# Kernel optimization log

Measured on AMD Instinct MI355X. Metric: run time of the kernel, lower is better.

The kernel has to match this reference:

```python
import jax
import jax.numpy as jnp
import numpy as np
import math

KNN = 16
DIST_THRESH = 0.03


def setup_inputs() -> dict:
    key = jax.random.key(0)
    ks = jax.random.split(key, 7)
    B, N, M = 2, 8192, 8192
    Din, D = 64, 64
    feature1 = jax.random.normal(ks[0], (B, N, Din), dtype=jnp.float32)
    xyz1 = jax.random.uniform(ks[1], (B, N, 3), dtype=jnp.float32)
    xyz2 = jax.random.uniform(ks[2], (B, M, 3), dtype=jnp.float32)
    Wp = jax.random.normal(ks[3], (Din, D), dtype=jnp.float32) * 0.05
    bp = jnp.zeros((D,), dtype=jnp.float32)
    W1 = jax.random.normal(ks[4], (3, D), dtype=jnp.float32) * 0.05
    b1 = jnp.zeros((D,), dtype=jnp.float32)
    W2 = jax.random.normal(ks[5], (D, D), dtype=jnp.float32) * 0.05
    b2 = jnp.zeros((D,), dtype=jnp.float32)
    return {"feature1": feature1, "xyz1": xyz1, "xyz2": xyz2,
            "Wp": Wp, "bp": bp, "W1": W1, "b1": b1, "W2": W2, "b2": b2}


def reference(feature1, xyz1, xyz2, Wp, bp, W1, b1, W2, b2):
    # prefix linear: [B,N,Din] -> [B,N,D]
    f = feature1 @ Wp + bp

    # knn_point: squared pairwise distance from queries xyz2 to points xyz1
    # d2: [B, M, N]
    d2 = (jnp.sum(xyz2 * xyz2, axis=-1)[:, :, None]
          + jnp.sum(xyz1 * xyz1, axis=-1)[:, None, :]
          - 2.0 * jnp.einsum('bmd,bnd->bmn', xyz2, xyz1))
    neg_d, idx = jax.lax.top_k(-d2, KNN)        # smallest-k, ascending
    dist = -neg_d                                # [B, M, KNN]

    min_distance = dist[:, :, 0]                 # [B, M]
    weight = jnp.where(min_distance > DIST_THRESH, 10.0, 1.0).astype(f.dtype)

    # index_points: per-batch gather of neighbor features / coords
    g_feature = jax.vmap(lambda a, i: a[i])(f, idx)      # [B, M, KNN, D]
    g_xyz = jax.vmap(lambda a, i: a[i])(xyz1, idx)       # [B, M, KNN, 3]
    g_xyz = g_xyz - xyz2[:, :, None, :]                  # relative coords

    # fc_position MLP: 3 -> D -> D
    pw = jax.nn.relu(g_xyz @ W1 + b1) @ W2 + b2          # [B, M, KNN, D]

    # per-channel weighted reduction over KNN neighbors
    new_feature = jnp.einsum('bmkc,bmkc->bmc', pw, g_feature) / math.sqrt(KNN)
    return new_feature, weight
```

## Files before the change

### kernel.cpp

```cpp
#include <hip/hip_runtime.h>
#include <math.h>

#define B 2
#define N 8192
#define M 8192
#define D 64
#define KNN 16
#define BM (B * M)
#define GC 16
#define NC (GC * GC * GC)
#define NSC 64
#define WTMAX 192
#define CAP 20
#define TCAP 448

using frag_ab = __attribute__((ext_vector_type(8))) short;
using frag_cd = __attribute__((ext_vector_type(4))) float;

__device__ __forceinline__ short f2bf(float x) {
    unsigned u = __float_as_uint(x);
    u += 0x7fffu + ((u >> 16) & 1u);
    return (short)(u >> 16);
}

__device__ __forceinline__ float query_cutr(float qx, float qy, float qz) {
    int nc = ((qx < 0.16f) | (qx > 0.84f)) + ((qy < 0.16f) | (qy > 0.84f))
           + ((qz < 0.16f) | (qz > 0.84f));
    return nc == 0 ? 0.121f : nc == 1 ? 0.1525f : nc == 2 ? 0.1921f : 0.242f;
}

#define CHAIN_INS(VARR, IARR, DVAL, IVAL) do {                          \
    float _dd = (DVAL); int _ii = (IVAL);                               \
    _Pragma("unroll")                                                   \
    for (int _r = 0; _r < KNN; ++_r) {                                  \
        bool  _sm = _dd < VARR[_r];                                     \
        float _tv = VARR[_r]; int _ti = IARR[_r];                       \
        VARR[_r] = _sm ? _dd : _tv;  IARR[_r] = _sm ? _ii : _ti;        \
        _dd      = _sm ? _tv : _dd;  _ii      = _sm ? _ti : _ii;        \
    }                                                                   \
} while (0)
#define CHAIN_INSERT(DVAL, IVAL) CHAIN_INS(v, id, DVAL, IVAL)

#define BITONIC_ROUND(VARR, IARR, DL) do {                              \
    float _nv[KNN]; int _nid[KNN];                                      \
    _Pragma("unroll")                                                   \
    for (int _i = 0; _i < KNN; ++_i) {                                  \
        float _pv = __shfl_xor(VARR[KNN - 1 - _i], (DL), 64);           \
        int   _pi = __shfl_xor(IARR[KNN - 1 - _i], (DL), 64);           \
        bool _tk = VARR[_i] <= _pv;                                     \
        _nv[_i]  = _tk ? VARR[_i] : _pv;                                \
        _nid[_i] = _tk ? IARR[_i] : _pi;                                \
    }                                                                   \
    _Pragma("unroll")                                                   \
    for (int _st = 8; _st; _st >>= 1) {                                 \
        _Pragma("unroll")                                               \
        for (int _i = 0; _i < KNN; ++_i) {                              \
            if (!(_i & _st)) {                                          \
                int _j = _i | _st;                                      \
                bool _sw = _nv[_i] > _nv[_j];                           \
                float _ta = _sw ? _nv[_j] : _nv[_i];                    \
                float _tb = _sw ? _nv[_i] : _nv[_j];                    \
                int _ia = _sw ? _nid[_j] : _nid[_i];                    \
                int _ib = _sw ? _nid[_i] : _nid[_j];                    \
                _nv[_i] = _ta; _nv[_j] = _tb;                           \
                _nid[_i] = _ia; _nid[_j] = _ib;                         \
            }                                                           \
        }                                                               \
    }                                                                   \
    _Pragma("unroll")                                                   \
    for (int _i = 0; _i < KNN; ++_i) { VARR[_i] = _nv[_i]; IARR[_i] = _nid[_i]; } \
} while (0)

#define KPROC(PV, TV) do {                                              \
    float _dx = (PV).x - qx, _dy = (PV).y - qy, _dz = (PV).z - qz;      \
    float _dv = fmaf(_dx, _dx, fmaf(_dy, _dy, _dz * _dz));              \
    if (_dv < fcut) {                                                   \
        if (cnt < CAP) {                                                \
            ibuf[cnt][lane] = (unsigned short)(TV);                     \
            ++cnt;                                                      \
        } else {                                   \
            CHAIN_INSERT(_dv, __float_as_int((PV).w));                  \
        }                                                               \
    }                                                                   \
} while (0)

#define KFLUSH() do {                                                   \
    int _t = 0;                                                         \
    for (; _t + 4 <= cur; _t += 4) {                                    \
        float4 _q0 = tile[_t + 0], _q1 = tile[_t + 1];                  \
        float4 _q2 = tile[_t + 2], _q3 = tile[_t + 3];                  \
        KPROC(_q0, _t + 0); KPROC(_q1, _t + 1);                         \
        KPROC(_q2, _t + 2); KPROC(_q3, _t + 3);                         \
    }                                                                   \
    for (; _t < cur; ++_t) { float4 _q0 = tile[_t]; KPROC(_q0, _t); }   \
    int _mx = cnt;                                                      \
    _Pragma("unroll")                                                   \
    for (int _o = 32; _o; _o >>= 1)                                     \
        _mx = max(_mx, __shfl_xor(_mx, _o, 64));                        \
    _mx = __builtin_amdgcn_readfirstlane(_mx);                          \
    int _t2 = 0;                                                        \
    for (; _t2 + 2 <= _mx; _t2 += 2) {                                  \
        int _ta = (_t2     < cnt) ? (int)ibuf[_t2    ][lane] : 0;       \
        int _tb = (_t2 + 1 < cnt) ? (int)ibuf[_t2 + 1][lane] : 0;       \
        float4 _pa = tile[_ta], _pb = tile[_tb];   \
        float _dxa = _pa.x - qx, _dya = _pa.y - qy, _dza = _pa.z - qz;  \
        float _dva = fmaf(_dxa, _dxa, fmaf(_dya, _dya, _dza * _dza));   \
        if (_t2 < cnt && _dva < v[KNN - 1])                             \
            CHAIN_INSERT(_dva, __float_as_int(_pa.w));                  \
        float _dxb = _pb.x - qx, _dyb = _pb.y - qy, _dzb = _pb.z - qz;  \
        float _dvb = fmaf(_dxb, _dxb, fmaf(_dyb, _dyb, _dzb * _dzb));   \
        if (_t2 + 1 < cnt && _dvb < v[KNN - 1])                         \
            CHAIN_INSERT(_dvb, __float_as_int(_pb.w));                  \
    }                                                                   \
    for (; _t2 < _mx; ++_t2) {                                          \
        int _tp = (_t2 < cnt) ? (int)ibuf[_t2][lane] : 0;               \
        float4 _p = tile[_tp];                                          \
        float _dx = _p.x - qx, _dy = _p.y - qy, _dz = _p.z - qz;        \
        float _dv = fmaf(_dx, _dx, fmaf(_dy, _dy, _dz * _dz));          \
        if (_t2 < cnt && _dv < v[KNN - 1])                              \
            CHAIN_INSERT(_dv, __float_as_int(_p.w));                    \
    }                                                                   \
    cnt = 0; cur = 0;                                                   \
} while (0)

__global__ __launch_bounds__(256) void k_prep(const float* __restrict__ feat,
                                              const float* __restrict__ Wp,
                                              const float* __restrict__ bp,
                                              const float* __restrict__ xyz1,
                                              const float* __restrict__ xyz2,
                                              unsigned* __restrict__ pcount,
                                              unsigned* __restrict__ qcount,
                                              float* __restrict__ f) {
    if (blockIdx.x < 64) {
        int i = blockIdx.x * 256 + threadIdx.x;
        int b = i >> 13;
        const float* p = xyz1 + (size_t)i * 3;
        int cx = max(0, min(GC - 1, (int)(p[0] * GC)));
        int cy = max(0, min(GC - 1, (int)(p[1] * GC)));
        int cz = max(0, min(GC - 1, (int)(p[2] * GC)));
        atomicAdd(&pcount[b * NC + (cz * GC + cy) * GC + cx], 1u);
        const float* q = xyz2 + (size_t)i * 3;
        int qx = max(0, min(GC - 1, (int)(q[0] * GC)));
        int qy = max(0, min(GC - 1, (int)(q[1] * GC)));
        int qz = max(0, min(GC - 1, (int)(q[2] * GC)));
        int sc = ((qz >> 2) * 4 + (qy >> 2)) * 4 + (qx >> 2);
        atomicAdd(&qcount[b * NSC + sc], 1u);
    }
    int c  = threadIdx.x & 63;
    int wv = threadIdx.x >> 6;
    int row0 = blockIdx.x * 32 + wv * 8;
    float wp[64];
#pragma unroll
    for (int d = 0; d < 64; ++d) wp[d] = Wp[d * 64 + c];
    float bpc = bp[c];
    float fv[8], acc[8];
#pragma unroll
    for (int r = 0; r < 8; ++r) {
        fv[r]  = feat[(size_t)(row0 + r) * 64 + c];
        acc[r] = bpc;
    }
#pragma unroll
    for (int d = 0; d < 64; ++d) {
#pragma unroll
        for (int r = 0; r < 8; ++r)
            acc[r] = fmaf(__shfl(fv[r], d, 64), wp[d], acc[r]);
    }
#pragma unroll
    for (int r = 0; r < 8; ++r)
        f[(size_t)(row0 + r) * 64 + c] = acc[r];
}

__global__ __launch_bounds__(256) void k_scan(const unsigned* __restrict__ pcount,
                                              const unsigned* __restrict__ qcount,
                                              unsigned* __restrict__ pstart,
                                              unsigned* __restrict__ pcur,
                                              unsigned* __restrict__ qcur,
                                              int* __restrict__ wtab,
                                              int* __restrict__ ntab) {
    __shared__ unsigned wsum[4];
    int blk = blockIdx.x;
    if (blk < 2) {
        int b = blk;
        int t = threadIdx.x;
        int base = b * NC + t * 16;
        unsigned c[16]; unsigned tsum = 0;
#pragma unroll
        for (int k = 0; k < 16; ++k) { c[k] = pcount[base + k]; tsum += c[k]; }
        int lane = t & 63, wv = t >> 6;
        unsigned x = tsum;
#pragma unroll
        for (int off = 1; off < 64; off <<= 1) {
            unsigned y = __shfl_up(x, off, 64);
            if (lane >= off) x += y;
        }
        if (lane == 63) wsum[wv] = x;
        __syncthreads();
        unsigned pre = 0;
        for (int k2 = 0; k2 < wv; ++k2) pre += wsum[k2];
        unsigned run = pre + x - tsum;
#pragma unroll
        for (int k = 0; k < 16; ++k) {
            pstart[base + k] = run; pcur[base + k] = run; run += c[k];
        }
    } else {
        int b = blk - 2;
        if (threadIdx.x >= 64) return;
        int lane = threadIdx.x;
        int c = (int)qcount[b * NSC + lane];
        int x = c;
#pragma unroll
        for (int off = 1; off < 64; off <<= 1) {
            int y = __shfl_up(x, off, 64);
            if (lane >= off) x += y;
        }
        int run = x - c;
        qcur[b * NSC + lane] = (unsigned)run;
        int ne = (c + 63) >> 6;
        int e = ne;
#pragma unroll
        for (int off = 1; off < 64; off <<= 1) {
            int y = __shfl_up(e, off, 64);
            if (lane >= off) e += y;
        }
        int eoff = e - ne;
        for (int j = 0; j < ne; ++j)
            wtab[b * WTMAX + eoff + j] = ((run + j * 64) << 7) | min(64, c - j * 64);
        if (lane == 63) ntab[b] = eoff + ne;
    }
}

__global__ __launch_bounds__(256) void k_scatter(const float* __restrict__ xyz1,
                                                 const float* __restrict__ xyz2,
                                                 unsigned* __restrict__ pcur,
                                                 unsigned* __restrict__ qcur,
                                                 float4* __restrict__ spts,
                                                 int* __restrict__ sidx,
                                                 float4* __restrict__ squery) {
    int i = blockIdx.x * 256 + threadIdx.x;
    int b = i >> 13;
    const float* p = xyz1 + (size_t)i * 3;
    float x = p[0], y = p[1], z = p[2];
    int cx = max(0, min(GC - 1, (int)(x * GC)));
    int cy = max(0, min(GC - 1, (int)(y * GC)));
    int cz = max(0, min(GC - 1, (int)(z * GC)));
    unsigned pos = atomicAdd(&pcur[b * NC + (cz * GC + cy) * GC + cx], 1u);
    spts[(size_t)b * N + pos] = make_float4(x, y, z, fmaf(x, x, fmaf(y, y, z * z)));
    sidx[(size_t)b * N + pos] = i & (N - 1);

    const float* q = xyz2 + (size_t)i * 3;
    float qx = q[0], qy = q[1], qz = q[2];
    int ax = max(0, min(GC - 1, (int)(qx * GC)));
    int ay = max(0, min(GC - 1, (int)(qy * GC)));
    int az = max(0, min(GC - 1, (int)(qz * GC)));
    int sc = ((az >> 2) * 4 + (ay >> 2)) * 4 + (ax >> 2);
    unsigned qpos = atomicAdd(&qcur[b * NSC + sc], 1u);
    squery[(size_t)b * M + qpos] = make_float4(qx, qy, qz, __int_as_float(i));
}

template <int NSLT>
__global__ __launch_bounds__(64) void k_knn(const float4* __restrict__ spts,
                                            const float4* __restrict__ squery,
                                            const unsigned* __restrict__ pstart,
                                            const unsigned* __restrict__ pcount,
                                            const int* __restrict__ wtab,
                                            const int* __restrict__ ntab,
                                            float* __restrict__ part_d,
                                            int* __restrict__ part_i) {
    __shared__ float4         tile[TCAP];
    __shared__ unsigned short ibuf[CAP][64];
    int bid = blockIdx.x;
    int b   = bid / (WTMAX * NSLT);
    int rem = bid - b * (WTMAX * NSLT);
    int ti  = rem / NSLT;
    int s   = rem % NSLT;
    if (ti >= ntab[b]) return;
    int e = wtab[b * WTMAX + ti];
    int qnum = e & 127, qoff = (e >> 7) & 0x3FFF;
    int lane = threadIdx.x;

    int sl = lane < qnum ? lane : qnum - 1;
    float4 q4 = squery[(size_t)b * M + qoff + sl];
    float qx = q4.x, qy = q4.y, qz = q4.z;
    float cutr = query_cutr(qx, qy, qz);
    float fcut = cutr * cutr;

    int lx0 = max(0, (int)floorf((qx - cutr) * GC));
    int lx1 = min(GC - 1, (int)floorf((qx + cutr) * GC));
    int ly0 = max(0, (int)floorf((qy - cutr) * GC));
    int ly1 = min(GC - 1, (int)floorf((qy + cutr) * GC));
    int lz0 = max(0, (int)floorf((qz - cutr) * GC));
    int lz1 = min(GC - 1, (int)floorf((qz + cutr) * GC));
#pragma unroll
    for (int off = 1; off < 64; off <<= 1) {
        lx0 = min(lx0, __shfl_xor(lx0, off, 64));
        lx1 = max(lx1, __shfl_xor(lx1, off, 64));
        ly0 = min(ly0, __shfl_xor(ly0, off, 64));
        ly1 = max(ly1, __shfl_xor(ly1, off, 64));
        lz0 = min(lz0, __shfl_xor(lz0, off, 64));
        lz1 = max(lz1, __shfl_xor(lz1, off, 64));
    }
    int bx0 = __builtin_amdgcn_readfirstlane(lx0);
    int bx1 = __builtin_amdgcn_readfirstlane(lx1);
    int by0 = __builtin_amdgcn_readfirstlane(ly0);
    int by1 = __builtin_amdgcn_readfirstlane(ly1);
    int bz0 = __builtin_amdgcn_readfirstlane(lz0);
    int bz1 = __builtin_amdgcn_readfirstlane(lz1);

    float v[KNN]; int id[KNN];
#pragma unroll
    for (int r = 0; r < KNN; ++r) { v[r] = 3.4e38f; id[r] = 0; }
    int cnt = 0, cur = 0;
    int pb = b * N, cb = b * NC;
    int xspan = bx1 - bx0;

    int ny = by1 - by0 + 1;
    int nrows = (bz1 - bz0 + 1) * ny;
    int myrows = (s < nrows) ? ((nrows - 1 - s) / NSLT + 1) : 0;
    int stj = 0, enj = 0;
    {
        int rj = s + NSLT * lane;
        if (lane < myrows) {
            int dz = rj / ny;
            int dy = rj - dz * ny;
            int codeL = cb + ((bz0 + dz) * GC + (by0 + dy)) * GC + bx0;
            stj = (int)pstart[codeL];
            enj = (int)pstart[codeL + xspan] + (int)pcount[codeL + xspan];
        }
    }
    for (int j = 0; j < myrows; ++j) {
        int st = __builtin_amdgcn_readfirstlane(__shfl(stj, j, 64));
        int en = __builtin_amdgcn_readfirstlane(__shfl(enj, j, 64));
        int len = en - st;
        if (cur + len > TCAP) KFLUSH();
        for (int u = lane; u < len; u += 64) {
            float4 p = spts[pb + st + u];
            p.w = __int_as_float(st + u);
            tile[cur + u] = p;
        }
        cur += len;
    }
    KFLUSH();

    if (lane < qnum) {
        size_t base = ((size_t)(b * M + qoff + lane) * NSLT + s) * KNN;
        float4* pd = (float4*)(part_d + base);
        int4*   pi = (int4*)(part_i + base);
#pragma unroll
        for (int r4 = 0; r4 < 4; ++r4) {
            pd[r4] = make_float4(v[r4 * 4 + 0], v[r4 * 4 + 1],
                                 v[r4 * 4 + 2], v[r4 * 4 + 3]);
            pi[r4] = make_int4(id[r4 * 4 + 0], id[r4 * 4 + 1],
                               id[r4 * 4 + 2], id[r4 * 4 + 3]);
        }
    }
}

template <int NSLT>
__global__ __launch_bounds__(256, 4) void k_merge(const float4* __restrict__ squery,
                                                  const float* __restrict__ part_d,
                                                  const int* __restrict__ part_i,
                                                  const int* __restrict__ sidx,
                                                  const float4* __restrict__ spts,
                                                  int* __restrict__ idx_out,
                                                  float* __restrict__ w_out) {
    constexpr int GS  = NSLT;
    constexpr int QPW = 64 / GS;
    int tid = threadIdx.x;
    int l   = tid & 63;
    int wv  = tid >> 6;
    int g   = l / GS;
    int gl  = l % GS;
    int sqid = blockIdx.x * (QPW * 4) + wv * QPW + g;
    int b = sqid >> 13;

    float v[KNN]; int id[KNN];
    {
        size_t base = ((size_t)sqid * GS + gl) * KNN;
        const float4* pd = (const float4*)(part_d + base);
        const int4*   pi = (const int4*)(part_i + base);
#pragma unroll
        for (int r4 = 0; r4 < 4; ++r4) {
            float4 dv = pd[r4]; int4 iv = pi[r4];
            v[r4 * 4 + 0] = dv.x; v[r4 * 4 + 1] = dv.y;
            v[r4 * 4 + 2] = dv.z; v[r4 * 4 + 3] = dv.w;
            id[r4 * 4 + 0] = iv.x; id[r4 * 4 + 1] = iv.y;
            id[r4 * 4 + 2] = iv.z; id[r4 * 4 + 3] = iv.w;
        }
    }
#pragma unroll
    for (int dl = 1; dl < GS; dl <<= 1)
        BITONIC_ROUND(v, id, dl);

    float4 q4 = squery[sqid];
    float cutr = query_cutr(q4.x, q4.y, q4.z);
    bool miss = !(v[KNN - 1] < cutr * cutr * 0.9999f);
    int gq = __float_as_int(q4.w);
    if (!miss) {
        if (gl == 0) w_out[gq] = (v[0] > 0.03f) ? 10.0f : 1.0f;
#pragma unroll
        for (int rr = 0; rr < (KNN + GS - 1) / GS; ++rr) {
            int r = gl + rr * GS;
            if (r < KNN) {
                int myid = 0;
#pragma unroll
                for (int k = 0; k < KNN; ++k) if (r == k) myid = id[k];
                idx_out[(size_t)r * BM + sqid] = sidx[b * N + myid];
            }
        }
    }

    unsigned long long mmask = __ballot(miss && gl == 0);
    while (mmask) {
        int ml = __ffsll(mmask) - 1;
        mmask &= mmask - 1;
        int msq = blockIdx.x * (QPW * 4) + wv * QPW + ml / GS;
        int mb = msq >> 13;
        float4 mq = squery[msq];
        float fv2[KNN]; int fi2[KNN];
#pragma unroll
        for (int r = 0; r < KNN; ++r) { fv2[r] = 3.4e38f; fi2[r] = 0; }
        for (int t = l; t < N; t += 64) {
            float4 p = spts[(size_t)mb * N + t];
            float dx = p.x - mq.x, dy = p.y - mq.y, dz = p.z - mq.z;
            float dv = fmaf(dx, dx, fmaf(dy, dy, dz * dz));
            if (dv < fv2[KNN - 1]) CHAIN_INS(fv2, fi2, dv, t);
        }
        BITONIC_ROUND(fv2, fi2, 1);
        BITONIC_ROUND(fv2, fi2, 2);
        BITONIC_ROUND(fv2, fi2, 4);
        BITONIC_ROUND(fv2, fi2, 8);
        BITONIC_ROUND(fv2, fi2, 16);
        BITONIC_ROUND(fv2, fi2, 32);
        int mgq = __float_as_int(mq.w);
        if (l == 0) w_out[mgq] = (fv2[0] > 0.03f) ? 10.0f : 1.0f;
        if (l < 16) {
            int myid = 0;
#pragma unroll
            for (int r = 0; r < KNN; ++r) if (l == r) myid = fi2[r];
            idx_out[(size_t)l * BM + msq] = sidx[mb * N + myid];
        }
    }
}

__global__ __launch_bounds__(256) void k_final(const float4* __restrict__ squery,
                                               const int* __restrict__ idxs,
                                               const float* __restrict__ xyz1,
                                               const float* __restrict__ f,
                                               const float* __restrict__ W1,
                                               const float* __restrict__ b1,
                                               const float* __restrict__ W2,
                                               const float* __restrict__ b2,
                                               float* __restrict__ out) {
    __shared__ __align__(16) unsigned short hT[4][16][72];
    int tid = threadIdx.x;
    int l   = tid & 63;
    int wv  = tid >> 6;
    int ln  = l & 15, lg = l >> 4;
    int mq  = __builtin_amdgcn_readfirstlane(blockIdx.x * 4 + wv);
    int bb  = mq >> 13;
    float4 q4 = squery[mq];
    int gq = __float_as_int(q4.w);
    float qx = q4.x, qy = q4.y, qz = q4.z;

    int nk[KNN];
#pragma unroll
    for (int k = 0; k < KNN; ++k)
        nk[k] = idxs[(size_t)k * BM + mq];

    frag_ab bfrag[4][2];
#pragma unroll
    for (int t = 0; t < 4; ++t)
#pragma unroll
        for (int s = 0; s < 2; ++s) {
            frag_ab bv;
#pragma unroll
            for (int j = 0; j < 8; ++j)
                bv[j] = f2bf(W2[(lg * 8 + j + 32 * s) * 64 + t * 16 + ln]);
            bfrag[t][s] = bv;
        }

    float w10 = W1[l], w11 = W1[64 + l], w12 = W1[128 + l], b1c = b1[l];

#pragma unroll
    for (int k = 0; k < KNN; ++k) {
        const float* p = xyz1 + ((size_t)bb * N + nk[k]) * 3;
        float gx = p[0] - qx, gy = p[1] - qy, gz = p[2] - qz;
        float t = fmaf(gx, w10, b1c);
        t = fmaf(gy, w11, t);
        t = fmaf(gz, w12, t);
        hT[wv][k][l] = (unsigned short)f2bf(fmaxf(t, 0.f));
    }

    frag_cd acc[4];
#pragma unroll
    for (int t = 0; t < 4; ++t) acc[t] = (frag_cd){0.f, 0.f, 0.f, 0.f};
#pragma unroll
    for (int s = 0; s < 2; ++s) {
        frag_ab af = *(const frag_ab*)&hT[wv][ln][lg * 8 + 32 * s];
#pragma unroll
        for (int t = 0; t < 4; ++t)
            acc[t] = __builtin_amdgcn_mfma_f32_16x16x32_bf16(af, bfrag[t][s],
                                                             acc[t], 0, 0, 0);
    }

    int nk4[4];
#pragma unroll
    for (int i = 0; i < 4; ++i)
        nk4[i] = idxs[(size_t)(lg * 4 + i) * BM + mq];

#pragma unroll
    for (int t = 0; t < 4; ++t) {
        float b2c = b2[t * 16 + ln];
        float s = 0.f;
#pragma unroll
        for (int i = 0; i < 4; ++i) {
            float gf = f[((size_t)bb * N + nk4[i]) * 64 + t * 16 + ln];
            s = fmaf(acc[t][i] + b2c, gf, s);
        }
        s += __shfl_xor(s, 16, 64);
        s += __shfl_xor(s, 32, 64);
        if (lg == t)
            out[(size_t)gq * 64 + t * 16 + ln] = s * 0.25f;
    }
}

extern "C" void kernel_launch(void* const* d_in, const int* in_sizes, int n_in,
                              void* d_out, int out_size, void* d_ws, size_t ws_size,
                              hipStream_t stream) {
    const float* feature1 = (const float*)d_in[0];
    const float* xyz1     = (const float*)d_in[1];
    const float* xyz2     = (const float*)d_in[2];
    const float* Wp       = (const float*)d_in[3];
    const float* bp       = (const float*)d_in[4];
    const float* W1       = (const float*)d_in[5];
    const float* b1       = (const float*)d_in[6];
    const float* W2       = (const float*)d_in[7];
    const float* b2       = (const float*)d_in[8];
    float* out = (float*)d_out;

    char* w = (char*)d_ws;
    float4*   spts   = (float4*)w;    w += (size_t)B * N * 16;
    float4*   squery = (float4*)w;    w += (size_t)B * M * 16;
    float*    f      = (float*)w;     w += (size_t)B * N * D * 4;
    int*      sidx   = (int*)w;       w += (size_t)B * N * 4;
    unsigned* pcount = (unsigned*)w;  w += (size_t)B * NC * 4;
    unsigned* qcount = (unsigned*)w;  w += (size_t)B * NSC * 4;
    unsigned* pstart = (unsigned*)w;  w += (size_t)B * NC * 4;
    unsigned* pcur   = (unsigned*)w;  w += (size_t)B * NC * 4;
    unsigned* qcur   = (unsigned*)w;  w += (size_t)B * NSC * 4;
    int*      wtab   = (int*)w;       w += (size_t)B * WTMAX * 4;
    int*      ntab   = (int*)w;       w += 16;

    size_t used_fixed = (size_t)(w - (char*)d_ws);
    size_t per_slice  = (size_t)KNN * BM * 8;
    size_t idxf_bytes = (size_t)KNN * BM * 4;
    int nsl = (ws_size >= used_fixed + 16 * per_slice + idxf_bytes) ? 16 : 8;

    float*    partd  = (float*)w;     w += (size_t)nsl * KNN * BM * 4;
    int*      parti  = (int*)w;       w += (size_t)nsl * KNN * BM * 4;
    int*      idxf   = (int*)w;       w += idxf_bytes;
    float*    w_out  = out + (size_t)BM * D;

    hipMemsetAsync(pcount, 0, (size_t)(B * NC + B * NSC) * 4, stream);

    k_prep<<<B * N / 32, 256, 0, stream>>>(feature1, Wp, bp, xyz1, xyz2,
                                           pcount, qcount, f);
    k_scan<<<4, 256, 0, stream>>>(pcount, qcount, pstart, pcur, qcur, wtab, ntab);
    k_scatter<<<BM / 256, 256, 0, stream>>>(xyz1, xyz2, pcur, qcur, spts, sidx, squery);
    if (nsl == 16) {
        k_knn<16><<<B * WTMAX * 16, 64, 0, stream>>>(spts, squery, pstart, pcount,
                                                     wtab, ntab, partd, parti);
        k_merge<16><<<BM / 16, 256, 0, stream>>>(squery, partd, parti, sidx, spts,
                                                 idxf, w_out);
    } else {
        k_knn<8><<<B * WTMAX * 8, 64, 0, stream>>>(spts, squery, pstart, pcount,
                                                   wtab, ntab, partd, parti);
        k_merge<8><<<BM / 32, 256, 0, stream>>>(squery, partd, parti, sidx, spts,
                                                idxf, w_out);
    }
    k_final<<<BM / 4, 256, 0, stream>>>(squery, idxf, xyz1, f,
                                        W1, b1, W2, b2, out);
}
```

Measured before the change: 198.3 us.

## Replace LDS tile staging in kNN with register batches and readlane broadcast

```diff
diff --git a/kernel.cpp b/kernel.cpp
--- a/kernel.cpp
+++ b/kernel.cpp
@@ -11,8 +11,6 @@
 #define NC (GC * GC * GC)
 #define NSC 64
 #define WTMAX 192
-#define CAP 20
-#define TCAP 448
 
 using frag_ab = __attribute__((ext_vector_type(8))) short;
 using frag_cd = __attribute__((ext_vector_type(4))) float;
@@ -71,56 +69,32 @@
     for (int _i = 0; _i < KNN; ++_i) { VARR[_i] = _nv[_i]; IARR[_i] = _nid[_i]; } \
 } while (0)
 
-#define KPROC(PV, TV) do {                                              \
-    float _dx = (PV).x - qx, _dy = (PV).y - qy, _dz = (PV).z - qz;      \
-    float _dv = fmaf(_dx, _dx, fmaf(_dy, _dy, _dz * _dz));              \
-    if (_dv < fcut) {                                                   \
-        if (cnt < CAP) {                                                \
-            ibuf[cnt][lane] = (unsigned short)(TV);                     \
-            ++cnt;                                                      \
-        } else {                                   \
-            CHAIN_INSERT(_dv, __float_as_int((PV).w));                  \
-        }                                                               \
+__device__ __forceinline__ float rdlane_f(float x, int u) {
+    return __uint_as_float((unsigned)__builtin_amdgcn_readlane(
+        (int)__float_as_uint(x), u));
+}
+
+#define SCANB(CNT) do {                                                 \
+    for (int _u = 0; _u < (CNT); ++_u) {                                \
+        float _px = rdlane_f(preg.x, _u);                               \
+        float _py = rdlane_f(preg.y, _u);                               \
+        float _pz = rdlane_f(preg.z, _u);                               \
+        float _dx = _px - qx, _dy = _py - qy, _dz = _pz - qz;           \
+        float _dv = fmaf(_dx, _dx, fmaf(_dy, _dy, _dz * _dz));          \
+        if (_dv < fcut) cand |= 1ull << _u;                             \
     }                                                                   \
-} while (0)
-
-#define KFLUSH() do {                                                   \
-    int _t = 0;                                                         \
-    for (; _t + 4 <= cur; _t += 4) {                                    \
-        float4 _q0 = tile[_t + 0], _q1 = tile[_t + 1];                  \
-        float4 _q2 = tile[_t + 2], _q3 = tile[_t + 3];                  \
-        KPROC(_q0, _t + 0); KPROC(_q1, _t + 1);                         \
-        KPROC(_q2, _t + 2); KPROC(_q3, _t + 3);                         \
+    while (__ballot(cand != 0)) {                                       \
+        int _u2 = cand ? (int)(__ffsll((long long)cand) - 1) : 0;       \
+        float _gx = __shfl(preg.x, _u2, 64);                            \
+        float _gy = __shfl(preg.y, _u2, 64);                            \
+        float _gz = __shfl(preg.z, _u2, 64);                            \
+        float _gw = __shfl(preg.w, _u2, 64);                            \
+        float _dx = _gx - qx, _dy = _gy - qy, _dz = _gz - qz;           \
+        float _dv = fmaf(_dx, _dx, fmaf(_dy, _dy, _dz * _dz));          \
+        if (cand && _dv < v[KNN - 1])                                   \
+            CHAIN_INSERT(_dv, __float_as_int(_gw));                     \
+        cand &= cand - 1;                                               \
     }                                                                   \
-    for (; _t < cur; ++_t) { float4 _q0 = tile[_t]; KPROC(_q0, _t); }   \
-    int _mx = cnt;                                                      \
-    _Pragma("unroll")                                                   \
-    for (int _o = 32; _o; _o >>= 1)                                     \
-        _mx = max(_mx, __shfl_xor(_mx, _o, 64));                        \
-    _mx = __builtin_amdgcn_readfirstlane(_mx);                          \
-    int _t2 = 0;                                                        \
-    for (; _t2 + 2 <= _mx; _t2 += 2) {                                  \
-        int _ta = (_t2     < cnt) ? (int)ibuf[_t2    ][lane] : 0;       \
-        int _tb = (_t2 + 1 < cnt) ? (int)ibuf[_t2 + 1][lane] : 0;       \
-        float4 _pa = tile[_ta], _pb = tile[_tb];   \
-        float _dxa = _pa.x - qx, _dya = _pa.y - qy, _dza = _pa.z - qz;  \
-        float _dva = fmaf(_dxa, _dxa, fmaf(_dya, _dya, _dza * _dza));   \
-        if (_t2 < cnt && _dva < v[KNN - 1])                             \
-            CHAIN_INSERT(_dva, __float_as_int(_pa.w));                  \
-        float _dxb = _pb.x - qx, _dyb = _pb.y - qy, _dzb = _pb.z - qz;  \
-        float _dvb = fmaf(_dxb, _dxb, fmaf(_dyb, _dyb, _dzb * _dzb));   \
-        if (_t2 + 1 < cnt && _dvb < v[KNN - 1])                         \
-            CHAIN_INSERT(_dvb, __float_as_int(_pb.w));                  \
-    }                                                                   \
-    for (; _t2 < _mx; ++_t2) {                                          \
-        int _tp = (_t2 < cnt) ? (int)ibuf[_t2][lane] : 0;               \
-        float4 _p = tile[_tp];                                          \
-        float _dx = _p.x - qx, _dy = _p.y - qy, _dz = _p.z - qz;        \
-        float _dv = fmaf(_dx, _dx, fmaf(_dy, _dy, _dz * _dz));          \
-        if (_t2 < cnt && _dv < v[KNN - 1])                              \
-            CHAIN_INSERT(_dv, __float_as_int(_p.w));                    \
-    }                                                                   \
-    cnt = 0; cur = 0;                                                   \
 } while (0)
 
 __global__ __launch_bounds__(256) void k_prep(const float* __restrict__ feat,
@@ -266,8 +240,6 @@
                                             const int* __restrict__ ntab,
                                             float* __restrict__ part_d,
                                             int* __restrict__ part_i) {
-    __shared__ float4         tile[TCAP];
-    __shared__ unsigned short ibuf[CAP][64];
     int bid = blockIdx.x;
     int b   = bid / (WTMAX * NSLT);
     int rem = bid - b * (WTMAX * NSLT);
@@ -309,7 +281,6 @@
     float v[KNN]; int id[KNN];
 #pragma unroll
     for (int r = 0; r < KNN; ++r) { v[r] = 3.4e38f; id[r] = 0; }
-    int cnt = 0, cur = 0;
     int pb = b * N, cb = b * NC;
     int xspan = bx1 - bx0;
 
@@ -327,19 +298,27 @@
             enj = (int)pstart[codeL + xspan] + (int)pcount[codeL + xspan];
         }
     }
+
+    unsigned long long cand = 0;
+    float4 preg = make_float4(3.4e38f, 3.4e38f, 3.4e38f, 0.f);
+    int cur = 0;
     for (int j = 0; j < myrows; ++j) {
         int st = __builtin_amdgcn_readfirstlane(__shfl(stj, j, 64));
         int en = __builtin_amdgcn_readfirstlane(__shfl(enj, j, 64));
         int len = en - st;
-        if (cur + len > TCAP) KFLUSH();
-        for (int u = lane; u < len; u += 64) {
-            float4 p = spts[pb + st + u];
-            p.w = __int_as_float(st + u);
-            tile[cur + u] = p;
-        }
-        cur += len;
-    }
-    KFLUSH();
+        while (len > 0) {
+            int take = min(len, 64 - cur);
+            if (lane >= cur && lane < cur + take) {
+                int addr = st + (lane - cur);
+                float4 p = spts[pb + addr];
+                p.w = __int_as_float(addr);
+                preg = p;
+            }
+            cur += take; st += take; len -= take;
+            if (cur == 64) { SCANB(64); cur = 0; }
+        }
+    }
+    if (cur > 0) SCANB(cur);
 
     if (lane < qnum) {
         size_t base = ((size_t)(b * M + qoff + lane) * NSLT + s) * KNN;
```

After: 203.9 us. 2.9% more time.
